# Performance work log

Measured on AMD Instinct MI355X. Metric: run time of the kernel, lower is better.

Reference implementation:

```python
import jax, jax.numpy as jnp
import numpy as np

N_USERS = 50000
N_PRODS = 50000
N_NODES = N_USERS + N_PRODS
N_EDGES = 600000
UD, PD, H, O = 64, 100, 128, 16


def _gcn_conv(x, W, b, src, dst, n):
    """PyG GCNConv: linear transform, add self-loops, sym-normalized scatter-add."""
    x = x @ W                                    # [n, H]
    loop = jnp.arange(n, dtype=src.dtype)
    src = jnp.concatenate([src, loop])
    dst = jnp.concatenate([dst, loop])
    deg = jax.ops.segment_sum(jnp.ones_like(dst, dtype=x.dtype), dst, num_segments=n)
    dinv = jnp.where(deg > 0, jax.lax.rsqrt(deg), 0.0)
    norm = dinv[src] * dinv[dst]                 # [E+n]
    msg = x[src] * norm[:, None]                 # gather + scale
    out = jax.ops.segment_sum(msg, dst, num_segments=n)
    return out + b


def setup_inputs() -> dict:
    key = jax.random.key(0)
    ks = jax.random.split(key, 16)
    s = 0.05
    return {
        "user_feats": jax.random.normal(ks[0], (N_USERS, UD), dtype=jnp.float32),
        "prod_feats": jax.random.normal(ks[1], (N_PRODS, PD), dtype=jnp.float32),
        "edge_index": jax.random.randint(ks[2], (2, N_EDGES), 0, N_NODES, dtype=jnp.int64),
        "Wu": jax.random.normal(ks[3], (UD, H), dtype=jnp.float32) * s,
        "bu": jnp.zeros((H,), dtype=jnp.float32),
        "Wp": jax.random.normal(ks[4], (PD, H), dtype=jnp.float32) * s,
        "bp": jnp.zeros((H,), dtype=jnp.float32),
        "W1": jax.random.normal(ks[5], (H, H), dtype=jnp.float32) * s,
        "b1": jnp.zeros((H,), dtype=jnp.float32),
        "W2": jax.random.normal(ks[6], (H, H), dtype=jnp.float32) * s,
        "b2": jnp.zeros((H,), dtype=jnp.float32),
        "W3": jax.random.normal(ks[7], (H, H), dtype=jnp.float32) * s,
        "b3": jnp.zeros((H,), dtype=jnp.float32),
        "Wo": jax.random.normal(ks[8], (H, O), dtype=jnp.float32) * s,
        "bo": jnp.zeros((O,), dtype=jnp.float32),
    }


def reference(user_feats, prod_feats, edge_index, Wu, bu, Wp, bp,
              W1, b1, W2, b2, W3, b3, Wo, bo):
    src, dst = edge_index[0], edge_index[1]
    user_x = user_feats @ Wu + bu
    prod_x = prod_feats @ Wp + bp
    x = jnp.concatenate([user_x, prod_x], axis=0)   # [N_NODES, H]
    x = jax.nn.relu(_gcn_conv(x, W1, b1, src, dst, N_NODES))
    # dropout p=0.6 is identity in eval mode
    x = jax.nn.relu(_gcn_conv(x, W2, b2, src, dst, N_NODES))
    x = jax.nn.relu(_gcn_conv(x, W3, b3, src, dst, N_NODES))
    return x @ Wo + bo                              # [N_NODES, O]
```

## Files before the change

### kernel.cpp

```cpp
#include <hip/hip_runtime.h>
#include <hip/hip_fp16.h>

#define NU 50000
#define NP 50000
#define NN 100000
#define NE 600000
#define H  128
#define O  16

typedef __attribute__((ext_vector_type(8))) _Float16 half8;
typedef __attribute__((ext_vector_type(4))) float f32x4;

__global__ void k_init(int* __restrict__ cnt, int* __restrict__ cursor, int n) {
    int i = blockIdx.x * blockDim.x + threadIdx.x;
    if (i < n) { cnt[i] = 0; cursor[i] = 0; }
}

__global__ void k_count(const int* __restrict__ dst, int* __restrict__ cnt, int E) {
    int e = blockIdx.x * blockDim.x + threadIdx.x;
    if (e < E) atomicAdd(&cnt[dst[e]], 1);
}

#define SCAN_TPB 256
#define SCAN_VPT 4
#define SCAN_CHUNK (SCAN_TPB * SCAN_VPT)

__global__ void k_scan1(const int* __restrict__ in, int* __restrict__ out,
                        int* __restrict__ bsums, float* __restrict__ dinv, int n) {
    __shared__ int sh[SCAN_TPB];
    int t = threadIdx.x, b = blockIdx.x;
    int base = b * SCAN_CHUNK + t * SCAN_VPT;
    int v[SCAN_VPT]; int s = 0;
#pragma unroll
    for (int i = 0; i < SCAN_VPT; i++) {
        int idx = base + i;
        v[i] = (idx < n) ? in[idx] : 0;
        if (idx < n) dinv[idx] = rsqrtf((float)(v[i] + 1));
        s += v[i];
    }
    sh[t] = s; __syncthreads();
    for (int off = 1; off < SCAN_TPB; off <<= 1) {
        int x = (t >= off) ? sh[t - off] : 0;
        __syncthreads();
        sh[t] += x;
        __syncthreads();
    }
    int run = (t > 0) ? sh[t - 1] : 0;
    if (t == SCAN_TPB - 1) bsums[b] = sh[t];
#pragma unroll
    for (int i = 0; i < SCAN_VPT; i++) {
        int idx = base + i;
        if (idx < n) out[idx] = run;
        run += v[i];
    }
}

__global__ void k_scan2(int* __restrict__ bsums, int nb, int* __restrict__ total) {
    __shared__ int sh[128];
    int t = threadIdx.x;
    int v = (t < nb) ? bsums[t] : 0;
    sh[t] = v; __syncthreads();
    for (int off = 1; off < 128; off <<= 1) {
        int x = (t >= off) ? sh[t - off] : 0;
        __syncthreads();
        sh[t] += x;
        __syncthreads();
    }
    if (t < nb) bsums[t] = sh[t] - v;
    if (t == 127) *total = sh[127];
}

__global__ void k_scan3(int* __restrict__ out, const int* __restrict__ bsums, int n) {
    int idx = blockIdx.x * blockDim.x + threadIdx.x;
    if (idx < n) out[idx] += bsums[idx / SCAN_CHUNK];
}

__global__ void k_fill(const int* __restrict__ src, const int* __restrict__ dst,
                       const int* __restrict__ offs, int* __restrict__ cursor,
                       const float* __restrict__ dinv,
                       int2* __restrict__ epack, int E) {
    int e = blockIdx.x * blockDim.x + threadIdx.x;
    if (e < E) {
        int s = src[e], d = dst[e];
        int p = offs[d] + atomicAdd(&cursor[d], 1);
        int2 r;
        r.x = s;
        r.y = __float_as_int(dinv[s] * dinv[d]);
        epack[p] = r;
    }
}

__global__ void k_wprep_all(const float* __restrict__ Wu, const float* __restrict__ Wp,
                            const float* __restrict__ W1, const float* __restrict__ W2,
                            const float* __restrict__ W3, const float* __restrict__ Wo,
                            __half* __restrict__ whU, __half* __restrict__ wlU,
                            __half* __restrict__ whP, __half* __restrict__ wlP,
                            __half* __restrict__ wh1, __half* __restrict__ wl1,
                            __half* __restrict__ wh2, __half* __restrict__ wl2,
                            __half* __restrict__ wh3, __half* __restrict__ wl3,
                            __half* __restrict__ whO, __half* __restrict__ wlO) {
    int idx = blockIdx.x * blockDim.x + threadIdx.x;
    const float* W; __half *Wh, *Wl; int K, KPAD, NC;
    if      (idx <  8192) {              W = Wu; Wh = whU; Wl = wlU; K =  64; KPAD =  64; NC = 128; }
    else if (idx < 24576) { idx -=  8192; W = Wp; Wh = whP; Wl = wlP; K = 100; KPAD = 128; NC = 128; }
    else if (idx < 40960) { idx -= 24576; W = W1; Wh = wh1; Wl = wl1; K = 128; KPAD = 128; NC = 128; }
    else if (idx < 57344) { idx -= 40960; W = W2; Wh = wh2; Wl = wl2; K = 128; KPAD = 128; NC = 128; }
    else if (idx < 73728) { idx -= 57344; W = W3; Wh = wh3; Wl = wl3; K = 128; KPAD = 128; NC = 128; }
    else if (idx < 75776) { idx -= 73728; W = Wo; Wh = whO; Wl = wlO; K = 128; KPAD = 128; NC =  16; }
    else return;
    int n = idx / KPAD, k = idx - n * KPAD;
    float x = (k < K) ? W[k * NC + n] * 16.0f : 0.0f;
    __half h = __float2half_rn(x);
    __half l = __float2half_rn(x - __half2float(h));
    Wh[idx] = h; Wl[idx] = l;
}

template <typename AT, int K, int KPAD, int MI, int NOUT, bool BIAS, bool F32OUT>
__launch_bounds__(256)
__global__ void k_gemm_reg(const AT* __restrict__ X,
                           const __half* __restrict__ Wh, const __half* __restrict__ Wl,
                           const float* __restrict__ bias, void* __restrict__ Cout,
                           int M, int orow0) {
    constexpr int KS = KPAD / 32;
    const int tid  = threadIdx.x;
    const int wid  = tid >> 6, lane = tid & 63;
    const int lm   = lane & 15, q = lane >> 4;
    const int gw   = blockIdx.x * 4 + wid;
    const int NT   = (M + 63) >> 6;
    int tile, c0;
    if constexpr (MI == 4) { tile = gw >> 1; c0 = (gw & 1) * 64; }
    else                   { tile = gw;      c0 = 0; }
    if (tile >= NT) return;
    const int n0 = tile * 64;

    half8 wh[MI][KS], wl[MI][KS];
#pragma unroll
    for (int mi = 0; mi < MI; mi++)
#pragma unroll
        for (int ks = 0; ks < KS; ks++) {
            const size_t b = (size_t)(c0 + mi * 16 + lm) * KPAD + ks * 32 + q * 8;
            wh[mi][ks] = *(const half8*)&Wh[b];
            wl[mi][ks] = *(const half8*)&Wl[b];
        }

    f32x4 acc[4][MI];
#pragma unroll
    for (int ni = 0; ni < 4; ni++)
#pragma unroll
        for (int mi = 0; mi < MI; mi++) acc[ni][mi] = (f32x4)0.0f;

#pragma unroll
    for (int ni = 0; ni < 4; ni++) {
        const int node = n0 + ni * 16 + lm;
        half8 xf[KS];
        if (node < M) {
            if constexpr (sizeof(AT) == 2) {
#pragma unroll
                for (int ks = 0; ks < KS; ks++)
                    xf[ks] = *(const half8*)((const __half*)X + (size_t)node * KPAD + ks * 32 + q * 8);
            } else {
                const float* xp = (const float*)X + (size_t)node * K;
#pragma unroll
                for (int ks = 0; ks < KS; ks++) {
                    const int kb = ks * 32 + q * 8;
                    if (kb + 8 <= K) {
                        float4 v0 = *(const float4*)(xp + kb);
                        float4 v1 = *(const float4*)(xp + kb + 4);
                        xf[ks][0] = (_Float16)v0.x; xf[ks][1] = (_Float16)v0.y;
                        xf[ks][2] = (_Float16)v0.z; xf[ks][3] = (_Float16)v0.w;
                        xf[ks][4] = (_Float16)v1.x; xf[ks][5] = (_Float16)v1.y;
                        xf[ks][6] = (_Float16)v1.z; xf[ks][7] = (_Float16)v1.w;
                    } else {
#pragma unroll
                        for (int j = 0; j < 8; j++) {
                            int k = kb + j;
                            xf[ks][j] = (k < K) ? (_Float16)xp[k] : (_Float16)0.0f;
                        }
                    }
                }
            }
        } else {
#pragma unroll
            for (int ks = 0; ks < KS; ks++)
#pragma unroll
                for (int j = 0; j < 8; j++) xf[ks][j] = (_Float16)0.0f;
        }
#pragma unroll
        for (int ks = 0; ks < KS; ks++)
#pragma unroll
            for (int mi = 0; mi < MI; mi++) {
                acc[ni][mi] = __builtin_amdgcn_mfma_f32_16x16x32_f16(wh[mi][ks], xf[ks], acc[ni][mi], 0, 0, 0);
                acc[ni][mi] = __builtin_amdgcn_mfma_f32_16x16x32_f16(wl[mi][ks], xf[ks], acc[ni][mi], 0, 0, 0);
            }
    }

#pragma unroll
    for (int ni = 0; ni < 4; ni++) {
        const int node = n0 + ni * 16 + lm;
        if (node >= M) continue;
#pragma unroll
        for (int mi = 0; mi < MI; mi++) {
            const int cb = c0 + mi * 16 + q * 4;
            float4 bv = BIAS ? *(const float4*)&bias[cb] : make_float4(0.f, 0.f, 0.f, 0.f);
            float v0 = fmaf(acc[ni][mi][0], 0.0625f, bv.x);
            float v1 = fmaf(acc[ni][mi][1], 0.0625f, bv.y);
            float v2 = fmaf(acc[ni][mi][2], 0.0625f, bv.z);
            float v3 = fmaf(acc[ni][mi][3], 0.0625f, bv.w);
            if constexpr (F32OUT) {
                *(float4*)((float*)Cout + (size_t)(orow0 + node) * NOUT + cb) =
                    make_float4(v0, v1, v2, v3);
            } else {
                __half2 h0 = __floats2half2_rn(v0, v1);
                __half2 h1 = __floats2half2_rn(v2, v3);
                uint2 o; o.x = *(unsigned*)&h0; o.y = *(unsigned*)&h1;
                *(uint2*)((__half*)Cout + (size_t)(orow0 + node) * NOUT + cb) = o;
            }
        }
    }
}

__launch_bounds__(256)
__global__ void k_aggregate(const __half* __restrict__ y, const int* __restrict__ offs,
                            const int2* __restrict__ epack,
                            const float* __restrict__ dinv, const float* __restrict__ bias,
                            __half* __restrict__ out) {
    const int node = __builtin_amdgcn_readfirstlane(blockIdx.x * 4 + (threadIdx.x >> 6));
    const int l    = threadIdx.x & 63;
    const int e0 = offs[node], e1 = offs[node + 1];

    const __half2* y2 = (const __half2*)y;
    float a0x = 0.f, a0y = 0.f, a1x = 0.f, a1y = 0.f;
    float a2x = 0.f, a2y = 0.f, a3x = 0.f, a3y = 0.f;

    int e = e0;
    for (; e + 4 <= e1; e += 4) {
        int2 p0 = epack[e];
        int2 p1 = epack[e + 1];
        int2 p2 = epack[e + 2];
        int2 p3 = epack[e + 3];
        int   s0 = __builtin_amdgcn_readfirstlane(p0.x);
        int   s1 = __builtin_amdgcn_readfirstlane(p1.x);
        int   s2 = __builtin_amdgcn_readfirstlane(p2.x);
        int   s3 = __builtin_amdgcn_readfirstlane(p3.x);
        float w0 = __int_as_float(__builtin_amdgcn_readfirstlane(p0.y));
        float w1 = __int_as_float(__builtin_amdgcn_readfirstlane(p1.y));
        float w2 = __int_as_float(__builtin_amdgcn_readfirstlane(p2.y));
        float w3 = __int_as_float(__builtin_amdgcn_readfirstlane(p3.y));
        __half2 v0 = y2[(size_t)s0 * 64 + l];
        __half2 v1 = y2[(size_t)s1 * 64 + l];
        __half2 v2 = y2[(size_t)s2 * 64 + l];
        __half2 v3 = y2[(size_t)s3 * 64 + l];
        const _Float16* h0 = (const _Float16*)&v0;
        const _Float16* h1 = (const _Float16*)&v1;
        const _Float16* h2 = (const _Float16*)&v2;
        const _Float16* h3 = (const _Float16*)&v3;
        a0x = fmaf((float)h0[0], w0, a0x); a0y = fmaf((float)h0[1], w0, a0y);
        a1x = fmaf((float)h1[0], w1, a1x); a1y = fmaf((float)h1[1], w1, a1y);
        a2x = fmaf((float)h2[0], w2, a2x); a2y = fmaf((float)h2[1], w2, a2y);
        a3x = fmaf((float)h3[0], w3, a3x); a3y = fmaf((float)h3[1], w3, a3y);
    }
    for (; e < e1; e++) {
        int2 p0 = epack[e];
        int   s0 = __builtin_amdgcn_readfirstlane(p0.x);
        float w0 = __int_as_float(__builtin_amdgcn_readfirstlane(p0.y));
        __half2 v0 = y2[(size_t)s0 * 64 + l];
        const _Float16* h0 = (const _Float16*)&v0;
        a0x = fmaf((float)h0[0], w0, a0x);
        a0y = fmaf((float)h0[1], w0, a0y);
    }

    float accx = (a0x + a1x) + (a2x + a3x);
    float accy = (a0y + a1y) + (a2y + a3y);

    const float di2 = dinv[node] * dinv[node];
    __half2 sv = y2[(size_t)node * 64 + l];
    const _Float16* sp = (const _Float16*)&sv;
    float2 bv = *(const float2*)&bias[2 * l];
    float rx = fmaf((float)sp[0], di2, accx) + bv.x;
    float ry = fmaf((float)sp[1], di2, accy) + bv.y;
    ((__half2*)out)[(size_t)node * 64 + l] =
        __floats2half2_rn(fmaxf(rx, 0.f), fmaxf(ry, 0.f));
}

extern "C" void kernel_launch(void* const* d_in, const int* in_sizes, int n_in,
                              void* d_out, int out_size, void* d_ws, size_t ws_size,
                              hipStream_t stream) {
    const float* user = (const float*)d_in[0];
    const float* prod = (const float*)d_in[1];
    const int*   eidx = (const int*)  d_in[2];
    const int*   edst = eidx + NE;
    const int*   esrc_in = eidx;
    const float* Wu = (const float*)d_in[3];
    const float* bu = (const float*)d_in[4];
    const float* Wp = (const float*)d_in[5];
    const float* bp = (const float*)d_in[6];
    const float* W1 = (const float*)d_in[7];
    const float* b1 = (const float*)d_in[8];
    const float* W2 = (const float*)d_in[9];
    const float* b2 = (const float*)d_in[10];
    const float* W3 = (const float*)d_in[11];
    const float* b3 = (const float*)d_in[12];
    const float* Wo = (const float*)d_in[13];
    const float* bo = (const float*)d_in[14];
    float* out = (float*)d_out;

    char* ws = (char*)d_ws;
    size_t p = 0;
    auto alloc = [&](size_t bytes) -> void* {
        void* r = ws + p;
        p += (bytes + 255) & ~(size_t)255;
        return r;
    };
    __half* xA   = (__half*)alloc((size_t)NN * H * 2);
    __half* xB   = (__half*)alloc((size_t)NN * H * 2);
    int*   cnt   = (int*)  alloc((size_t)NN * 4);
    int*   cursor= (int*)  alloc((size_t)NN * 4);
    int*   offs  = (int*)  alloc((size_t)(NN + 1) * 4);
    float* dinv  = (float*)alloc((size_t)NN * 4);
    int2*  epack = (int2*) alloc((size_t)NE * 8);
    int*   bsums = (int*)  alloc(128 * 4);
    __half* whU = (__half*)alloc(128 * 64 * 2);
    __half* wlU = (__half*)alloc(128 * 64 * 2);
    __half* whP = (__half*)alloc(128 * 128 * 2);
    __half* wlP = (__half*)alloc(128 * 128 * 2);
    __half* wh1 = (__half*)alloc(128 * 128 * 2);
    __half* wl1 = (__half*)alloc(128 * 128 * 2);
    __half* wh2 = (__half*)alloc(128 * 128 * 2);
    __half* wl2 = (__half*)alloc(128 * 128 * 2);
    __half* wh3 = (__half*)alloc(128 * 128 * 2);
    __half* wl3 = (__half*)alloc(128 * 128 * 2);
    __half* whO = (__half*)alloc(16 * 128 * 2);
    __half* wlO = (__half*)alloc(16 * 128 * 2);

    const int NBLK = (NN + SCAN_CHUNK - 1) / SCAN_CHUNK;

    k_wprep_all<<<(75776 + 255) / 256, 256, 0, stream>>>(
        Wu, Wp, W1, W2, W3, Wo,
        whU, wlU, whP, wlP, wh1, wl1, wh2, wl2, wh3, wl3, whO, wlO);

    k_init <<<(NN + 255) / 256, 256, 0, stream>>>(cnt, cursor, NN);
    k_count<<<(NE + 255) / 256, 256, 0, stream>>>(edst, cnt, NE);
    k_scan1<<<NBLK, SCAN_TPB, 0, stream>>>(cnt, offs, bsums, dinv, NN);
    k_scan2<<<1, 128, 0, stream>>>(bsums, NBLK, offs + NN);
    k_scan3<<<(NN + 255) / 256, 256, 0, stream>>>(offs, bsums, NN);
    k_fill <<<(NE + 255) / 256, 256, 0, stream>>>(esrc_in, edst, offs, cursor, dinv,
                                                  epack, NE);

    {
        int ntU = (NU + 63) / 64, blkU = (ntU * 2 + 3) / 4;
        k_gemm_reg<float,  64,  64, 4, 128, true, false><<<blkU, 256, 0, stream>>>(user, whU, wlU, bu, xA, NU, 0);
        int ntP = (NP + 63) / 64, blkP = (ntP * 2 + 3) / 4;
        k_gemm_reg<float, 100, 128, 4, 128, true, false><<<blkP, 256, 0, stream>>>(prod, whP, wlP, bp, xA, NP, NU);
    }

    const int ntN  = (NN + 63) / 64;
    const int blkG = (ntN * 2 + 3) / 4;
    const int blkO = (ntN + 3) / 4;

    k_gemm_reg<__half, 128, 128, 4, 128, false, false><<<blkG, 256, 0, stream>>>(xA, wh1, wl1, nullptr, xB, NN, 0);
    k_aggregate<<<NN / 4, 256, 0, stream>>>(xB, offs, epack, dinv, b1, xA);
    k_gemm_reg<__half, 128, 128, 4, 128, false, false><<<blkG, 256, 0, stream>>>(xA, wh2, wl2, nullptr, xB, NN, 0);
    k_aggregate<<<NN / 4, 256, 0, stream>>>(xB, offs, epack, dinv, b2, xA);
    k_gemm_reg<__half, 128, 128, 4, 128, false, false><<<blkG, 256, 0, stream>>>(xA, wh3, wl3, nullptr, xB, NN, 0);
    k_aggregate<<<NN / 4, 256, 0, stream>>>(xB, offs, epack, dinv, b3, xA);

    k_gemm_reg<__half, 128, 128, 1, 16, true, true><<<blkO, 256, 0, stream>>>(xA, whO, wlO, bo, out, NN, 0);
}
```

Before: 315.6 us.

## Fuse setup kernels, record atomic ranks for CSR fill, split-wave aggregate

Merges weight prep with counter zeroing, stores each edge's atomic rank during counting so the fill needs no second atomic, and drops the scan3 pass by adding block sums at use sites. It also fuses the two input-projection GEMMs into one launch. The aggregate kernel now has each half-wave handle a different edge with 4-wide fp16 loads, then combines the halves with a cross-lane shuffle. This cuts launch count and atomic traffic, and raises memory-level parallelism in the gather, at the cost of an extra rank array and predicated tail loads.

```diff
diff --git a/kernel.cpp b/kernel.cpp
--- a/kernel.cpp
+++ b/kernel.cpp
@@ -9,16 +9,43 @@
 #define O  16
 
 typedef __attribute__((ext_vector_type(8))) _Float16 half8;
+typedef __attribute__((ext_vector_type(4))) _Float16 h4v;
 typedef __attribute__((ext_vector_type(4))) float f32x4;
 
-__global__ void k_init(int* __restrict__ cnt, int* __restrict__ cursor, int n) {
-    int i = blockIdx.x * blockDim.x + threadIdx.x;
-    if (i < n) { cnt[i] = 0; cursor[i] = 0; }
-}
-
-__global__ void k_count(const int* __restrict__ dst, int* __restrict__ cnt, int E) {
+__global__ void k_prep(const float* __restrict__ Wu, const float* __restrict__ Wp,
+                       const float* __restrict__ W1, const float* __restrict__ W2,
+                       const float* __restrict__ W3, const float* __restrict__ Wo,
+                       __half* __restrict__ whU, __half* __restrict__ wlU,
+                       __half* __restrict__ whP, __half* __restrict__ wlP,
+                       __half* __restrict__ wh1, __half* __restrict__ wl1,
+                       __half* __restrict__ wh2, __half* __restrict__ wl2,
+                       __half* __restrict__ wh3, __half* __restrict__ wl3,
+                       __half* __restrict__ whO, __half* __restrict__ wlO,
+                       int* __restrict__ cnt) {
+    int idx = blockIdx.x * blockDim.x + threadIdx.x;
+    if (idx >= 75776) {
+        int i = idx - 75776;
+        if (i < NN) cnt[i] = 0;
+        return;
+    }
+    const float* W; __half *Wh, *Wl; int K, KPAD, NC;
+    if      (idx <  8192) {              W = Wu; Wh = whU; Wl = wlU; K =  64; KPAD =  64; NC = 128; }
+    else if (idx < 24576) { idx -=  8192; W = Wp; Wh = whP; Wl = wlP; K = 100; KPAD = 128; NC = 128; }
+    else if (idx < 40960) { idx -= 24576; W = W1; Wh = wh1; Wl = wl1; K = 128; KPAD = 128; NC = 128; }
+    else if (idx < 57344) { idx -= 40960; W = W2; Wh = wh2; Wl = wl2; K = 128; KPAD = 128; NC = 128; }
+    else if (idx < 73728) { idx -= 57344; W = W3; Wh = wh3; Wl = wl3; K = 128; KPAD = 128; NC = 128; }
+    else                  { idx -= 73728; W = Wo; Wh = whO; Wl = wlO; K = 128; KPAD = 128; NC =  16; }
+    int n = idx / KPAD, k = idx - n * KPAD;
+    float x = (k < K) ? W[k * NC + n] * 16.0f : 0.0f;
+    __half h = __float2half_rn(x);
+    __half l = __float2half_rn(x - __half2float(h));
+    Wh[idx] = h; Wl[idx] = l;
+}
+
+__global__ void k_count(const int* __restrict__ dst, int* __restrict__ cnt,
+                        int* __restrict__ rank, int E) {
     int e = blockIdx.x * blockDim.x + threadIdx.x;
-    if (e < E) atomicAdd(&cnt[dst[e]], 1);
+    if (e < E) rank[e] = atomicAdd(&cnt[dst[e]], 1);
 }
 
 #define SCAN_TPB 256
@@ -55,7 +82,7 @@
     }
 }
 
-__global__ void k_scan2(int* __restrict__ bsums, int nb, int* __restrict__ total) {
+__global__ void k_scan2(int* __restrict__ bsums, int nb) {
     __shared__ int sh[128];
     int t = threadIdx.x;
     int v = (t < nb) ? bsums[t] : 0;
@@ -67,22 +94,16 @@
         __syncthreads();
     }
     if (t < nb) bsums[t] = sh[t] - v;
-    if (t == 127) *total = sh[127];
-}
-
-__global__ void k_scan3(int* __restrict__ out, const int* __restrict__ bsums, int n) {
-    int idx = blockIdx.x * blockDim.x + threadIdx.x;
-    if (idx < n) out[idx] += bsums[idx / SCAN_CHUNK];
 }
 
 __global__ void k_fill(const int* __restrict__ src, const int* __restrict__ dst,
-                       const int* __restrict__ offs, int* __restrict__ cursor,
-                       const float* __restrict__ dinv,
+                       const int* __restrict__ offs, const int* __restrict__ bsums,
+                       const int* __restrict__ rank, const float* __restrict__ dinv,
                        int2* __restrict__ epack, int E) {
     int e = blockIdx.x * blockDim.x + threadIdx.x;
     if (e < E) {
         int s = src[e], d = dst[e];
-        int p = offs[d] + atomicAdd(&cursor[d], 1);
+        int p = offs[d] + bsums[d >> 10] + rank[e];
         int2 r;
         r.x = s;
         r.y = __float_as_int(dinv[s] * dinv[d]);
@@ -90,42 +111,17 @@
     }
 }
 
-__global__ void k_wprep_all(const float* __restrict__ Wu, const float* __restrict__ Wp,
-                            const float* __restrict__ W1, const float* __restrict__ W2,
-                            const float* __restrict__ W3, const float* __restrict__ Wo,
-                            __half* __restrict__ whU, __half* __restrict__ wlU,
-                            __half* __restrict__ whP, __half* __restrict__ wlP,
-                            __half* __restrict__ wh1, __half* __restrict__ wl1,
-                            __half* __restrict__ wh2, __half* __restrict__ wl2,
-                            __half* __restrict__ wh3, __half* __restrict__ wl3,
-                            __half* __restrict__ whO, __half* __restrict__ wlO) {
-    int idx = blockIdx.x * blockDim.x + threadIdx.x;
-    const float* W; __half *Wh, *Wl; int K, KPAD, NC;
-    if      (idx <  8192) {              W = Wu; Wh = whU; Wl = wlU; K =  64; KPAD =  64; NC = 128; }
-    else if (idx < 24576) { idx -=  8192; W = Wp; Wh = whP; Wl = wlP; K = 100; KPAD = 128; NC = 128; }
-    else if (idx < 40960) { idx -= 24576; W = W1; Wh = wh1; Wl = wl1; K = 128; KPAD = 128; NC = 128; }
-    else if (idx < 57344) { idx -= 40960; W = W2; Wh = wh2; Wl = wl2; K = 128; KPAD = 128; NC = 128; }
-    else if (idx < 73728) { idx -= 57344; W = W3; Wh = wh3; Wl = wl3; K = 128; KPAD = 128; NC = 128; }
-    else if (idx < 75776) { idx -= 73728; W = Wo; Wh = whO; Wl = wlO; K = 128; KPAD = 128; NC =  16; }
-    else return;
-    int n = idx / KPAD, k = idx - n * KPAD;
-    float x = (k < K) ? W[k * NC + n] * 16.0f : 0.0f;
-    __half h = __float2half_rn(x);
-    __half l = __float2half_rn(x - __half2float(h));
-    Wh[idx] = h; Wl[idx] = l;
-}
-
 template <typename AT, int K, int KPAD, int MI, int NOUT, bool BIAS, bool F32OUT>
-__launch_bounds__(256)
-__global__ void k_gemm_reg(const AT* __restrict__ X,
-                           const __half* __restrict__ Wh, const __half* __restrict__ Wl,
-                           const float* __restrict__ bias, void* __restrict__ Cout,
-                           int M, int orow0) {
+__device__ __forceinline__
+void gemm_body(const AT* __restrict__ X,
+               const __half* __restrict__ Wh, const __half* __restrict__ Wl,
+               const float* __restrict__ bias, void* __restrict__ Cout,
+               int M, int orow0, int vb) {
     constexpr int KS = KPAD / 32;
     const int tid  = threadIdx.x;
     const int wid  = tid >> 6, lane = tid & 63;
     const int lm   = lane & 15, q = lane >> 4;
-    const int gw   = blockIdx.x * 4 + wid;
+    const int gw   = vb * 4 + wid;
     const int NT   = (M + 63) >> 6;
     int tile, c0;
     if constexpr (MI == 4) { tile = gw >> 1; c0 = (gw & 1) * 64; }
@@ -219,67 +215,91 @@
     }
 }
 
+template <typename AT, int K, int KPAD, int MI, int NOUT, bool BIAS, bool F32OUT>
+__launch_bounds__(256)
+__global__ void k_gemm_reg(const AT* __restrict__ X,
+                           const __half* __restrict__ Wh, const __half* __restrict__ Wl,
+                           const float* __restrict__ bias, void* __restrict__ Cout,
+                           int M, int orow0) {
+    gemm_body<AT, K, KPAD, MI, NOUT, BIAS, F32OUT>(X, Wh, Wl, bias, Cout, M, orow0, blockIdx.x);
+}
+
+__launch_bounds__(256)
+__global__ void k_gemm_inputs(const float* __restrict__ user, const float* __restrict__ prod,
+                              const __half* __restrict__ whU, const __half* __restrict__ wlU,
+                              const __half* __restrict__ whP, const __half* __restrict__ wlP,
+                              const float* __restrict__ bu, const float* __restrict__ bp,
+                              void* __restrict__ xA, int blkU) {
+    if ((int)blockIdx.x < blkU)
+        gemm_body<float,  64,  64, 4, 128, true, false>(user, whU, wlU, bu, xA, NU, 0, blockIdx.x);
+    else
+        gemm_body<float, 100, 128, 4, 128, true, false>(prod, whP, wlP, bp, xA, NP, NU, blockIdx.x - blkU);
+}
+
 __launch_bounds__(256)
 __global__ void k_aggregate(const __half* __restrict__ y, const int* __restrict__ offs,
-                            const int2* __restrict__ epack,
+                            const int* __restrict__ bsums, const int2* __restrict__ epack,
                             const float* __restrict__ dinv, const float* __restrict__ bias,
                             __half* __restrict__ out) {
     const int node = __builtin_amdgcn_readfirstlane(blockIdx.x * 4 + (threadIdx.x >> 6));
-    const int l    = threadIdx.x & 63;
-    const int e0 = offs[node], e1 = offs[node + 1];
-
-    const __half2* y2 = (const __half2*)y;
-    float a0x = 0.f, a0y = 0.f, a1x = 0.f, a1y = 0.f;
-    float a2x = 0.f, a2y = 0.f, a3x = 0.f, a3y = 0.f;
-
-    int e = e0;
-    for (; e + 4 <= e1; e += 4) {
-        int2 p0 = epack[e];
-        int2 p1 = epack[e + 1];
-        int2 p2 = epack[e + 2];
-        int2 p3 = epack[e + 3];
-        int   s0 = __builtin_amdgcn_readfirstlane(p0.x);
-        int   s1 = __builtin_amdgcn_readfirstlane(p1.x);
-        int   s2 = __builtin_amdgcn_readfirstlane(p2.x);
-        int   s3 = __builtin_amdgcn_readfirstlane(p3.x);
-        float w0 = __int_as_float(__builtin_amdgcn_readfirstlane(p0.y));
-        float w1 = __int_as_float(__builtin_amdgcn_readfirstlane(p1.y));
-        float w2 = __int_as_float(__builtin_amdgcn_readfirstlane(p2.y));
-        float w3 = __int_as_float(__builtin_amdgcn_readfirstlane(p3.y));
-        __half2 v0 = y2[(size_t)s0 * 64 + l];
-        __half2 v1 = y2[(size_t)s1 * 64 + l];
-        __half2 v2 = y2[(size_t)s2 * 64 + l];
-        __half2 v3 = y2[(size_t)s3 * 64 + l];
-        const _Float16* h0 = (const _Float16*)&v0;
-        const _Float16* h1 = (const _Float16*)&v1;
-        const _Float16* h2 = (const _Float16*)&v2;
-        const _Float16* h3 = (const _Float16*)&v3;
-        a0x = fmaf((float)h0[0], w0, a0x); a0y = fmaf((float)h0[1], w0, a0y);
-        a1x = fmaf((float)h1[0], w1, a1x); a1y = fmaf((float)h1[1], w1, a1y);
-        a2x = fmaf((float)h2[0], w2, a2x); a2y = fmaf((float)h2[1], w2, a2y);
-        a3x = fmaf((float)h3[0], w3, a3x); a3y = fmaf((float)h3[1], w3, a3y);
-    }
-    for (; e < e1; e++) {
-        int2 p0 = epack[e];
-        int   s0 = __builtin_amdgcn_readfirstlane(p0.x);
-        float w0 = __int_as_float(__builtin_amdgcn_readfirstlane(p0.y));
-        __half2 v0 = y2[(size_t)s0 * 64 + l];
-        const _Float16* h0 = (const _Float16*)&v0;
-        a0x = fmaf((float)h0[0], w0, a0x);
-        a0y = fmaf((float)h0[1], w0, a0y);
-    }
-
-    float accx = (a0x + a1x) + (a2x + a3x);
-    float accy = (a0y + a1y) + (a2y + a3y);
+    const int l = threadIdx.x & 63;
+    const int h = l >> 5, j = l & 31;
+
+    int e0 = offs[node] + bsums[node >> 10];
+    int e1 = (node + 1 < NN) ? (offs[node + 1] + bsums[(node + 1) >> 10]) : NE;
+    e0 = __builtin_amdgcn_readfirstlane(e0);
+    e1 = __builtin_amdgcn_readfirstlane(e1);
+
+    const h4v* y4 = (const h4v*)y;
+    f32x4 acc0 = (f32x4)0.f, acc1 = (f32x4)0.f, acc2 = (f32x4)0.f, acc3 = (f32x4)0.f;
+    const int e1m1 = e1 - 1;
+
+    for (int e = e0; e < e1; e += 8) {
+        const int ee0 = e + 0 + h;
+        const int ee1 = e + 2 + h;
+        const int ee2 = e + 4 + h;
+        const int ee3 = e + 6 + h;
+        int2 p0 = epack[min(ee0, e1m1)];
+        int2 p1 = epack[min(ee1, e1m1)];
+        int2 p2 = epack[min(ee2, e1m1)];
+        int2 p3 = epack[min(ee3, e1m1)];
+        float w0 = (ee0 < e1) ? __int_as_float(p0.y) : 0.f;
+        float w1 = (ee1 < e1) ? __int_as_float(p1.y) : 0.f;
+        float w2 = (ee2 < e1) ? __int_as_float(p2.y) : 0.f;
+        float w3 = (ee3 < e1) ? __int_as_float(p3.y) : 0.f;
+        h4v v0 = y4[(size_t)p0.x * 32 + j];
+        h4v v1 = y4[(size_t)p1.x * 32 + j];
+        h4v v2 = y4[(size_t)p2.x * 32 + j];
+        h4v v3 = y4[(size_t)p3.x * 32 + j];
+        acc0[0] = fmaf((float)v0[0], w0, acc0[0]); acc0[1] = fmaf((float)v0[1], w0, acc0[1]);
+        acc0[2] = fmaf((float)v0[2], w0, acc0[2]); acc0[3] = fmaf((float)v0[3], w0, acc0[3]);
+        acc1[0] = fmaf((float)v1[0], w1, acc1[0]); acc1[1] = fmaf((float)v1[1], w1, acc1[1]);
+        acc1[2] = fmaf((float)v1[2], w1, acc1[2]); acc1[3] = fmaf((float)v1[3], w1, acc1[3]);
+        acc2[0] = fmaf((float)v2[0], w2, acc2[0]); acc2[1] = fmaf((float)v2[1], w2, acc2[1]);
+        acc2[2] = fmaf((float)v2[2], w2, acc2[2]); acc2[3] = fmaf((float)v2[3], w2, acc2[3]);
+        acc3[0] = fmaf((float)v3[0], w3, acc3[0]); acc3[1] = fmaf((float)v3[1], w3, acc3[1]);
+        acc3[2] = fmaf((float)v3[2], w3, acc3[2]); acc3[3] = fmaf((float)v3[3], w3, acc3[3]);
+    }
+
+    f32x4 s = (acc0 + acc1) + (acc2 + acc3);
+    float t0 = s[0] + __shfl_xor(s[0], 32, 64);
+    float t1 = s[1] + __shfl_xor(s[1], 32, 64);
+    float t2 = s[2] + __shfl_xor(s[2], 32, 64);
+    float t3 = s[3] + __shfl_xor(s[3], 32, 64);
 
     const float di2 = dinv[node] * dinv[node];
-    __half2 sv = y2[(size_t)node * 64 + l];
-    const _Float16* sp = (const _Float16*)&sv;
-    float2 bv = *(const float2*)&bias[2 * l];
-    float rx = fmaf((float)sp[0], di2, accx) + bv.x;
-    float ry = fmaf((float)sp[1], di2, accy) + bv.y;
-    ((__half2*)out)[(size_t)node * 64 + l] =
-        __floats2half2_rn(fmaxf(rx, 0.f), fmaxf(ry, 0.f));
+    h4v sv = y4[(size_t)node * 32 + j];
+    float4 bv = *(const float4*)&bias[4 * j];
+    float r0 = fmaf((float)sv[0], di2, t0) + bv.x;
+    float r1 = fmaf((float)sv[1], di2, t1) + bv.y;
+    float r2 = fmaf((float)sv[2], di2, t2) + bv.z;
+    float r3 = fmaf((float)sv[3], di2, t3) + bv.w;
+    if (l < 32) {
+        __half2 ha = __floats2half2_rn(fmaxf(r0, 0.f), fmaxf(r1, 0.f));
+        __half2 hb = __floats2half2_rn(fmaxf(r2, 0.f), fmaxf(r3, 0.f));
+        uint2 o; o.x = *(unsigned*)&ha; o.y = *(unsigned*)&hb;
+        *(uint2*)(out + (size_t)node * H + 4 * j) = o;
+    }
 }
 
 extern "C" void kernel_launch(void* const* d_in, const int* in_sizes, int n_in,
@@ -289,7 +309,7 @@
     const float* prod = (const float*)d_in[1];
     const int*   eidx = (const int*)  d_in[2];
     const int*   edst = eidx + NE;
-    const int*   esrc_in = eidx;
+    const int*   esrc = eidx;
     const float* Wu = (const float*)d_in[3];
     const float* bu = (const float*)d_in[4];
     const float* Wp = (const float*)d_in[5];
@@ -314,7 +334,7 @@
     __half* xA   = (__half*)alloc((size_t)NN * H * 2);
     __half* xB   = (__half*)alloc((size_t)NN * H * 2);
     int*   cnt   = (int*)  alloc((size_t)NN * 4);
-    int*   cursor= (int*)  alloc((size_t)NN * 4);
+    int*   rank  = (int*)  alloc((size_t)NE * 4);
     int*   offs  = (int*)  alloc((size_t)(NN + 1) * 4);
     float* dinv  = (float*)alloc((size_t)NN * 4);
     int2*  epack = (int2*) alloc((size_t)NE * 8);
@@ -334,23 +354,21 @@
 
     const int NBLK = (NN + SCAN_CHUNK - 1) / SCAN_CHUNK;
 
-    k_wprep_all<<<(75776 + 255) / 256, 256, 0, stream>>>(
+    k_prep<<<(75776 + NN + 255) / 256, 256, 0, stream>>>(
         Wu, Wp, W1, W2, W3, Wo,
-        whU, wlU, whP, wlP, wh1, wl1, wh2, wl2, wh3, wl3, whO, wlO);
-
-    k_init <<<(NN + 255) / 256, 256, 0, stream>>>(cnt, cursor, NN);
-    k_count<<<(NE + 255) / 256, 256, 0, stream>>>(edst, cnt, NE);
+        whU, wlU, whP, wlP, wh1, wl1, wh2, wl2, wh3, wl3, whO, wlO, cnt);
+
+    k_count<<<(NE + 255) / 256, 256, 0, stream>>>(edst, cnt, rank, NE);
     k_scan1<<<NBLK, SCAN_TPB, 0, stream>>>(cnt, offs, bsums, dinv, NN);
-    k_scan2<<<1, 128, 0, stream>>>(bsums, NBLK, offs + NN);
-    k_scan3<<<(NN + 255) / 256, 256, 0, stream>>>(offs, bsums, NN);
-    k_fill <<<(NE + 255) / 256, 256, 0, stream>>>(esrc_in, edst, offs, cursor, dinv,
+    k_scan2<<<1, 128, 0, stream>>>(bsums, NBLK);
+    k_fill <<<(NE + 255) / 256, 256, 0, stream>>>(esrc, edst, offs, bsums, rank, dinv,
                                                   epack, NE);
 
     {
-        int ntU = (NU + 63) / 64, blkU = (ntU * 2 + 3) / 4;
-        k_gemm_reg<float,  64,  64, 4, 128, true, false><<<blkU, 256, 0, stream>>>(user, whU, wlU, bu, xA, NU, 0);
-        int ntP = (NP + 63) / 64, blkP = (ntP * 2 + 3) / 4;
-        k_gemm_reg<float, 100, 128, 4, 128, true, false><<<blkP, 256, 0, stream>>>(prod, whP, wlP, bp, xA, NP, NU);
+        constexpr int ntU = (NU + 63) / 64, blkU = (ntU * 2 + 3) / 4;
+        constexpr int ntP = (NP + 63) / 64, blkP = (ntP * 2 + 3) / 4;
+        k_gemm_inputs<<<blkU + blkP, 256, 0, stream>>>(
+            user, prod, whU, wlU, whP, wlP, bu, bp, xA, blkU);
     }
 
     const int ntN  = (NN + 63) / 64;
@@ -358,11 +376,11 @@
     const int blkO = (ntN + 3) / 4;
 
     k_gemm_reg<__half, 128, 128, 4, 128, false, false><<<blkG, 256, 0, stream>>>(xA, wh1, wl1, nullptr, xB, NN, 0);
-    k_aggregate<<<NN / 4, 256, 0, stream>>>(xB, offs, epack, dinv, b1, xA);
+    k_aggregate<<<NN / 4, 256, 0, stream>>>(xB, offs, bsums, epack, dinv, b1, xA);
     k_gemm_reg<__half, 128, 128, 4, 128, false, false><<<blkG, 256, 0, stream>>>(xA, wh2, wl2, nullptr, xB, NN, 0);
-    k_aggregate<<<NN / 4, 256, 0, stream>>>(xB, offs, epack, dinv, b2, xA);
+    k_aggregate<<<NN / 4, 256, 0, stream>>>(xB, offs, bsums, epack, dinv, b2, xA);
     k_gemm_reg<__half, 128, 128, 4, 128, false, false><<<blkG, 256, 0, stream>>>(xA, wh3, wl3, nullptr, xB, NN, 0);
-    k_aggregate<<<NN / 4, 256, 0, stream>>>(xB, offs, epack, dinv, b3, xA);
+    k_aggregate<<<NN / 4, 256, 0, stream>>>(xB, offs, bsums, epack, dinv, b3, xA);
 
     k_gemm_reg<__half, 128, 128, 1, 16, true, true><<<blkO, 256, 0, stream>>>(xA, whO, wlO, bo, out, NN, 0);
 }
```

New measurement: 303.2 us. 1.04x faster.
